# Kernel tuning notes

Hardware: AMD Instinct MI355X
Metric: run time of the kernel (lower is better)

## Reference

```python
import jax, jax.numpy as jnp
import numpy as np

N = 50000      # nodes
E = 800000     # edges (before self loops)
F_IN = 16      # n_input_features
PRE = 32       # n_channels_preproc
C = 128        # n_channels
GH = 32        # edge_gate_hidden_dim
L = 5          # n_gnn_layers (tied weights)


def setup_inputs() -> dict:
    key = jax.random.key(0)
    ks = jax.random.split(key, 16)
    def w(k, shape):
        return jax.random.normal(k, shape, jnp.float32) * 0.05
    return dict(
        x=jax.random.normal(ks[0], (N, F_IN), jnp.float32),
        edge_index=jax.random.randint(ks[1], (2, E), 0, N),
        edge_attr=jax.random.normal(ks[2], (E, 1), jnp.float32),
        W_pre=w(ks[3], (F_IN, PRE)), b_pre=jnp.zeros((PRE,), jnp.float32),
        W_init=w(ks[4], (PRE, C)), b_init=jnp.zeros((C,), jnp.float32),
        W_g1=w(ks[5], (2 * C + 1, GH)), b_g1=jnp.zeros((GH,), jnp.float32),
        W_g2=w(ks[6], (GH, 1)), b_g2=jnp.zeros((1,), jnp.float32),
        W_z=w(ks[7], (2 * C, C)), b_z=jnp.zeros((C,), jnp.float32),
        W_r=w(ks[8], (2 * C, C)), b_r=jnp.zeros((C,), jnp.float32),
        W_h=w(ks[9], (2 * C, C)), b_h=jnp.zeros((C,), jnp.float32),
        W_f1=w(ks[10], (2 * C, C)), b_f1=jnp.zeros((C,), jnp.float32),
        W_f2=w(ks[11], (C, 2)), b_f2=jnp.zeros((2,), jnp.float32),
    )


def reference(x, edge_index, edge_attr,
              W_pre, b_pre, W_init, b_init,
              W_g1, b_g1, W_g2, b_g2,
              W_z, b_z, W_r, b_r, W_h, b_h,
              W_f1, b_f1, W_f2, b_f2):
    n = x.shape[0]
    # add self loops (fill_value=0.0 for edge_attr)
    sl = jnp.arange(n)
    row = jnp.concatenate([edge_index[0], sl])   # source (x_j)
    col = jnp.concatenate([edge_index[1], sl])   # target (x_i), aggregation index
    ea = jnp.concatenate([edge_attr, jnp.zeros((n, 1), x.dtype)], axis=0)
    # symmetric normalization from in-degree (degree of col, incl. self loops)
    deg = jax.ops.segment_sum(jnp.ones(col.shape[0], x.dtype), col, num_segments=n)
    dis = jnp.where(deg > 0, deg ** -0.5, 0.0)
    norm = (dis[row] * dis[col])[:, None]        # [E', 1]

    # preproc + initial node transform
    h = jax.nn.relu(x @ W_pre + b_pre)
    h0 = jax.nn.relu(h @ W_init + b_init)
    h = h0

    for _ in range(L):  # tied GGNN layers
        x_i = h[col]                              # gather target feats  [E', C]
        x_j = h[row]                              # gather source feats  [E', C]
        g_in = jnp.concatenate([x_i, x_j, ea], axis=-1)          # [E', 2C+1]
        gate = jax.nn.sigmoid(jax.nn.relu(g_in @ W_g1 + b_g1) @ W_g2 + b_g2)
        msg = gate * (norm * x_j)                                  # [E', C]
        aggr = jax.ops.segment_sum(msg, col, num_segments=n)       # scatter-add
        # GRU-style update
        za = jnp.concatenate([h, aggr], axis=-1)                   # [N, 2C]
        z = jax.nn.sigmoid(za @ W_z + b_z)
        r = jax.nn.sigmoid(za @ W_r + b_r)
        hc = jax.nn.relu(jnp.concatenate([r * h, aggr], axis=-1) @ W_h + b_h)
        h = (1.0 - z) * h + z * hc

    out = jnp.concatenate([h0, h], axis=-1)       # [N, 2C]
    out = jax.nn.relu(out @ W_f1 + b_f1)
    return out @ W_f2 + b_f2                      # [N, 2] logits (output_activation='none')
```

## Files before the change

### kernel.cpp

```cpp
#include <hip/hip_runtime.h>
#include <math.h>

#define NODES 50000
#define NEDGES 800000
#define ETOT (NEDGES + NODES)
#define FIN 16
#define PRE 32
#define C 128
#define GH 32
#define LAYERS 5
#define RECS 160
#define SCB 64
#define SCT 256
#define SCCH ((NODES + SCB*SCT - 1) / (SCB*SCT))

typedef _Float16 f16;
typedef f16 f16x8 __attribute__((ext_vector_type(8)));
typedef f16 f16x4 __attribute__((ext_vector_type(4)));
typedef f16 f16x2 __attribute__((ext_vector_type(2)));
typedef float f32x4 __attribute__((ext_vector_type(4)));

__device__ __forceinline__ float sigmoidf_(float x) { return 1.0f / (1.0f + __expf(-x)); }

__device__ __forceinline__ int swz_off(int row, int bytecol, int stride) {
    return row * stride + ((((bytecol) >> 4) ^ (row & 7)) << 4) + (bytecol & 15);
}

__device__ __forceinline__ int bperm(int c) { return 4 * (c & 7) + (c >> 3); }

__global__ void k_degree(const int* __restrict__ col, float* __restrict__ deg) {
    int e = blockIdx.x * blockDim.x + threadIdx.x;
    if (e < NEDGES) atomicAdd(&deg[col[e]], 1.0f);
}

__global__ __launch_bounds__(SCT) void k_scan1(const float* __restrict__ deg, int* __restrict__ bsum) {
    __shared__ int ws4[SCT / 64];
    int b = blockIdx.x, t = threadIdx.x;
    int lane = t & 63, wv = t >> 6;
    int base = (b * SCT + t) * SCCH;
    int sum = 0;
#pragma unroll
    for (int j = 0; j < SCCH; j++) {
        int i = base + j;
        if (i < NODES) sum += (int)deg[i] + 1;
    }
#pragma unroll
    for (int off = 32; off > 0; off >>= 1) sum += __shfl_xor(sum, off, 64);
    if (lane == 0) ws4[wv] = sum;
    __syncthreads();
    if (t == 0) {
        int tot = 0;
#pragma unroll
        for (int j = 0; j < SCT / 64; j++) tot += ws4[j];
        bsum[b] = tot;
    }
}

__global__ __launch_bounds__(64) void k_scan2(const int* __restrict__ bsum, int* __restrict__ bscan,
                                              int* __restrict__ start) {
    int t = threadIdx.x;
    int v = (t < SCB) ? bsum[t] : 0;
    int x = v;
#pragma unroll
    for (int off = 1; off < 64; off <<= 1) {
        int tt = __shfl_up(x, off, 64);
        if (t >= off) x += tt;
    }
    if (t < SCB) bscan[t] = x - v;
    if (t == SCB - 1) start[NODES] = x;
}

__global__ __launch_bounds__(SCT) void k_scan3(
    float* __restrict__ deg_dis, const int* __restrict__ bscan,
    int* __restrict__ start, int* __restrict__ cursor) {
    __shared__ int woff[SCT / 64];
    int b = blockIdx.x, t = threadIdx.x;
    int lane = t & 63, wv = t >> 6;
    int base = (b * SCT + t) * SCCH;
    int v[SCCH]; int sum = 0;
#pragma unroll
    for (int j = 0; j < SCCH; j++) {
        int i = base + j;
        v[j] = (i < NODES) ? (int)deg_dis[i] + 1 : 0;
        sum += v[j];
    }
    int x = sum;
#pragma unroll
    for (int off = 1; off < 64; off <<= 1) {
        int tt = __shfl_up(x, off, 64);
        if (lane >= off) x += tt;
    }
    int texcl = x - sum;
    if (lane == 63) woff[wv] = x;
    __syncthreads();
    int wbase = 0;
    for (int j = 0; j < wv; j++) wbase += woff[j];
    int run = bscan[b] + wbase + texcl;
#pragma unroll
    for (int j = 0; j < SCCH; j++) {
        int i = base + j;
        if (i < NODES) {
            start[i] = run; cursor[i] = run;
            deg_dis[i] = rsqrtf((float)v[j]);
        }
        run += v[j];
    }
}

__global__ __launch_bounds__(256) void k_csr(
    const int* __restrict__ eidx, const float* __restrict__ eattr,
    int* __restrict__ cursor,
    int* __restrict__ row_sorted, float* __restrict__ ea_sorted) {
    int e = blockIdx.x * blockDim.x + threadIdx.x;
    if (e >= ETOT) return;
    int r, ci; float ea;
    if (e < NEDGES) { r = eidx[e]; ci = eidx[NEDGES + e]; ea = eattr[e]; }
    else            { r = ci = e - NEDGES; ea = 0.0f; }
    int slot = atomicAdd(&cursor[ci], 1);
    row_sorted[slot] = r;
    ea_sorted[slot] = ea;
}

__global__ __launch_bounds__(256) void k_prep_w(
    const float* __restrict__ Wz, const float* __restrict__ Wr, const float* __restrict__ Wh,
    const float* __restrict__ Wg1, const float* __restrict__ Wf1,
    f16* __restrict__ WcatF, f16* __restrict__ WhtopF, f16* __restrict__ Wg1F,
    f16* __restrict__ Wf1F) {
    int t = blockIdx.x * 256 + threadIdx.x;
    int l = t & 63;
    int lr = l & 15, lh = l >> 4;
    if (t < 24 * 8 * 64) {
        int idx = t >> 6; int nt = idx >> 3, ks = idx & 7;
        int wv = nt / 6, ntl = nt % 6;
        int grp = ntl >> 1, pr = ntl & 1;
        int ncol = (2 * wv + pr) * 16 + lr;
        f16x8 v;
#pragma unroll
        for (int j = 0; j < 8; j++) {
            int k = ks * 32 + lh * 8 + j;
            float x;
            if (grp == 0)      x = Wz[k * 128 + ncol];
            else if (grp == 1) x = Wr[k * 128 + ncol];
            else               x = (k >= 128) ? Wh[k * 128 + ncol] : 0.0f;
            v[j] = (f16)x;
        }
        *(f16x8*)(WcatF + (size_t)t * 8) = v;
    } else if (t < 24 * 8 * 64 + 8 * 4 * 64) {
        int t2 = t - 24 * 8 * 64;
        int idx = t2 >> 6; int nt = idx >> 2, ks = idx & 3;
        int n = nt * 16 + lr;
        f16x8 v;
#pragma unroll
        for (int j = 0; j < 8; j++) {
            int k = ks * 32 + lh * 8 + j;
            v[j] = (f16)Wh[k * 128 + n];
        }
        *(f16x8*)(WhtopF + (size_t)t2 * 8) = v;
    } else if (t < 24 * 8 * 64 + 8 * 4 * 64 + 4 * 4 * 64) {
        int t3 = t - (24 * 8 * 64 + 8 * 4 * 64);
        int idx = t3 >> 6; int nt = idx >> 2, ks = idx & 3;
        int cg = nt * 16 + lr;
        f16x8 v;
#pragma unroll
        for (int j = 0; j < 8; j++) {
            int k = ks * 32 + lh * 8 + j;
            v[j] = (f16)((cg < 32) ? Wg1[k * GH + cg] : Wg1[(128 + k) * GH + (cg - 32)]);
        }
        *(f16x8*)(Wg1F + (size_t)t3 * 8) = v;
    } else if (t < 24 * 8 * 64 + 8 * 4 * 64 + 4 * 4 * 64 + 8 * 8 * 64) {
        int t4 = t - (24 * 8 * 64 + 8 * 4 * 64 + 4 * 4 * 64);
        int idx = t4 >> 6; int nt = idx >> 3, ks = idx & 7;
        int n = nt * 16 + lr;
        f16x8 v;
#pragma unroll
        for (int j = 0; j < 8; j++) {
            int k = ks * 32 + lh * 8 + j;
            v[j] = (f16)Wf1[k * 128 + n];
        }
        *(f16x8*)(Wf1F + (size_t)t4 * 8) = v;
    }
}

__global__ __launch_bounds__(256) void k_preproc(
    const float* __restrict__ x, const float* __restrict__ Wpre, const float* __restrict__ bpre,
    const float* __restrict__ Winit, const float* __restrict__ binit,
    f16* __restrict__ h0_16, f16* __restrict__ h16) {
    __shared__ float sWpre[FIN * PRE], sbpre[PRE], sWinit[PRE * C], sbinit[C];
    for (int i = threadIdx.x; i < FIN * PRE; i += blockDim.x) sWpre[i] = Wpre[i];
    for (int i = threadIdx.x; i < PRE; i += blockDim.x) sbpre[i] = bpre[i];
    for (int i = threadIdx.x; i < PRE * C; i += blockDim.x) sWinit[i] = Winit[i];
    for (int i = threadIdx.x; i < C; i += blockDim.x) sbinit[i] = binit[i];
    __syncthreads();
    int wave = (blockIdx.x * blockDim.x + threadIdx.x) >> 6;
    int lane = threadIdx.x & 63;
    if (wave >= NODES) return;
    float xk = (lane < FIN) ? x[(size_t)wave * FIN + lane] : 0.0f;
    float pre = (lane < PRE) ? sbpre[lane] : 0.0f;
#pragma unroll
    for (int i = 0; i < FIN; i++) {
        float xi = __shfl(xk, i, 64);
        pre = fmaf(xi, (lane < PRE) ? sWpre[i * PRE + lane] : 0.0f, pre);
    }
    pre = fmaxf(pre, 0.0f);
    int c = lane * 2;
    float a0 = sbinit[c], a1 = sbinit[c + 1];
#pragma unroll
    for (int j = 0; j < PRE; j++) {
        float pj = __shfl(pre, j, 64);
        a0 = fmaf(pj, sWinit[j * C + c], a0);
        a1 = fmaf(pj, sWinit[j * C + c + 1], a1);
    }
    a0 = fmaxf(a0, 0.0f); a1 = fmaxf(a1, 0.0f);
    f16x2 o; o[0] = (f16)a0; o[1] = (f16)a1;
    *(f16x2*)&h0_16[(size_t)wave * C + c] = o;
    *(f16x2*)&h16[(size_t)wave * C + c] = o;
}

__global__ __launch_bounds__(256) void k_gate0_mfma(
    const f16* __restrict__ h16, const float* __restrict__ dis,
    const f16* __restrict__ Wg1F, const float* __restrict__ bg1,
    float* __restrict__ A, f16* __restrict__ rec) {
    __shared__ f16 za[32 * 128];
    char* zaB = (char*)za;
    int tid = threadIdx.x;
    int l = tid & 63, w = tid >> 6;
    int lr = l & 15, lh = l >> 4;
    int n0 = blockIdx.x * 32;

    for (int p = tid; p < 32 * 16; p += 256) {
        int row = p >> 4, seg = p & 15;
        int gn = n0 + row;
        f16x8 v = {};
        if (gn < NODES) v = *(const f16x8*)(h16 + (size_t)gn * C + seg * 8);
        *(f16x8*)(zaB + swz_off(row, seg * 16, 256)) = v;
        if (gn < NODES) {
            float dn = dis[gn];
            f16x8 od;
#pragma unroll
            for (int j = 0; j < 8; j++) od[j] = (f16)((float)v[j] * dn);
            *(f16x8*)(rec + (size_t)gn * RECS + 32 + seg * 8) = od;
        }
    }
    __syncthreads();

    f32x4 acc3[2];
#pragma unroll
    for (int rt = 0; rt < 2; rt++)
#pragma unroll
        for (int j = 0; j < 4; j++) acc3[rt][j] = 0.0f;
#pragma unroll
    for (int ks = 0; ks < 4; ks++) {
        int kk = ks * 32 + lh * 8;
        f16x8 a0 = *(const f16x8*)(zaB + swz_off(lr,      kk * 2, 256));
        f16x8 a1 = *(const f16x8*)(zaB + swz_off(lr + 16, kk * 2, 256));
        f16x8 b = *(const f16x8*)(Wg1F + ((size_t)(w * 4 + ks) * 64 + l) * 8);
        acc3[0] = __builtin_amdgcn_mfma_f32_16x16x32_f16(a0, b, acc3[0], 0, 0, 0);
        acc3[1] = __builtin_amdgcn_mfma_f32_16x16x32_f16(a1, b, acc3[1], 0, 0, 0);
    }
    int col3 = w * 16 + lr;
#pragma unroll
    for (int rt = 0; rt < 2; rt++)
#pragma unroll
        for (int j = 0; j < 4; j++) {
            int row = rt * 16 + lh * 4 + j;
            int gn = n0 + row;
            if (gn < NODES) {
                float v = acc3[rt][j];
                if (col3 < 32) A[(size_t)gn * GH + bperm(col3)] = v + bg1[col3];
                else           rec[(size_t)gn * RECS + bperm(col3 - 32)] = (f16)v;
            }
        }
}

__global__ __launch_bounds__(256) void k_msg(
    const int* __restrict__ start, const int* __restrict__ row_sorted,
    const float* __restrict__ ea_sorted, const float* __restrict__ dis,
    const float* __restrict__ A, const f16* __restrict__ rec,
    const float* __restrict__ Wg1, const float* __restrict__ Wg2, const float* __restrict__ bg2,
    f16* __restrict__ aggr16) {
    int wid = (blockIdx.x * blockDim.x + threadIdx.x) >> 6;
    int lane = threadIdx.x & 63;
    if (wid >= NODES) return;
    int k8 = lane & 7;
    int q = lane >> 3;
    int s0 = start[wid], s1 = start[wid + 1];
    float4 a4 = *(const float4*)(A + (size_t)wid * GH + k8 * 4);
    const float* wg1e = Wg1 + 2 * C * GH;
    float wea0 = wg1e[k8], wea1 = wg1e[k8 + 8], wea2 = wg1e[k8 + 16], wea3 = wg1e[k8 + 24];
    float w20 = Wg2[k8], w21 = Wg2[k8 + 8], w22 = Wg2[k8 + 16], w23 = Wg2[k8 + 24];
    float b2 = bg2[0];
    float dci = dis[wid];
    float acc[16];
#pragma unroll
    for (int j = 0; j < 16; j++) acc[j] = 0.0f;

    int s = s0 + q;
    f16x8 ha0 = {}, hb0 = {};
    f16x4 bb0 = {};
    float ea0 = 0.0f;
    if (s < s1) {
        int r = row_sorted[s];
        ea0 = ea_sorted[s];
        const f16* rr = rec + (size_t)r * RECS;
        bb0 = *(const f16x4*)(rr + k8 * 4);
        ha0 = *(const f16x8*)(rr + 32 + k8 * 16);
        hb0 = *(const f16x8*)(rr + 32 + k8 * 16 + 8);
    }
    while (s < s1) {
        int s2 = s + 8;
        f16x8 ha1 = {}, hb1 = {};
        f16x4 bb1 = {};
        float ea1 = 0.0f;
        if (s2 < s1) {
            int r = row_sorted[s2];
            ea1 = ea_sorted[s2];
            const f16* rr = rec + (size_t)r * RECS;
            bb1 = *(const f16x4*)(rr + k8 * 4);
            ha1 = *(const f16x8*)(rr + 32 + k8 * 16);
            hb1 = *(const f16x8*)(rr + 32 + k8 * 16 + 8);
        }
        float t0 = fmaxf(a4.x + (float)bb0[0] + ea0 * wea0, 0.0f);
        float t1 = fmaxf(a4.y + (float)bb0[1] + ea0 * wea1, 0.0f);
        float t2 = fmaxf(a4.z + (float)bb0[2] + ea0 * wea2, 0.0f);
        float t3 = fmaxf(a4.w + (float)bb0[3] + ea0 * wea3, 0.0f);
        float p = t0 * w20;
        p = fmaf(t1, w21, p);
        p = fmaf(t2, w22, p);
        p = fmaf(t3, w23, p);
        p += __shfl_xor(p, 4, 8);
        p += __shfl_xor(p, 2, 8);
        p += __shfl_xor(p, 1, 8);
        float coef = sigmoidf_(p + b2);
#pragma unroll
        for (int j = 0; j < 8; j++) {
            acc[j]     = fmaf(coef, (float)ha0[j], acc[j]);
            acc[8 + j] = fmaf(coef, (float)hb0[j], acc[8 + j]);
        }
        ha0 = ha1; hb0 = hb1; bb0 = bb1; ea0 = ea1;
        s = s2;
    }
#pragma unroll
    for (int j = 0; j < 16; j++) {
        acc[j] += __shfl_xor(acc[j], 8, 64);
        acc[j] += __shfl_xor(acc[j], 16, 64);
        acc[j] += __shfl_xor(acc[j], 32, 64);
    }
    if (lane < 8) {
        f16x8 o1, o2;
#pragma unroll
        for (int j = 0; j < 8; j++) { o1[j] = (f16)(acc[j] * dci); o2[j] = (f16)(acc[8 + j] * dci); }
        *(f16x8*)(aggr16 + (size_t)wid * C + k8 * 16) = o1;
        *(f16x8*)(aggr16 + (size_t)wid * C + k8 * 16 + 8) = o2;
    }
}

__global__ __launch_bounds__(256) void k_update_mfma(
    f16* __restrict__ h16, const f16* __restrict__ aggr16, const float* __restrict__ dis,
    f16* __restrict__ rec,
    const f16* __restrict__ WcatF, const f16* __restrict__ WhtopF, const f16* __restrict__ Wg1F,
    const float* __restrict__ bz, const float* __restrict__ br, const float* __restrict__ bh,
    const float* __restrict__ bg1,
    float* __restrict__ A) {
    __shared__ f16 za[32 * 256];
    __shared__ f16 rhbuf[32 * 128];
    char* zaB = (char*)za;
    char* rhB = (char*)rhbuf;
    int tid = threadIdx.x;
    int l = tid & 63, w = tid >> 6;
    int lr = l & 15, lh = l >> 4;
    int n0 = blockIdx.x * 32;

    for (int p = tid; p < 32 * 16; p += 256) {
        int row = p >> 4, seg = p & 15;
        int gn = n0 + row;
        f16x8 v = {};
        if (gn < NODES) v = *(const f16x8*)(h16 + (size_t)gn * C + seg * 8);
        *(f16x8*)(zaB + swz_off(row, seg * 16, 512)) = v;
    }
    for (int p = tid; p < 32 * 16; p += 256) {
        int row = p >> 4, seg = p & 15;
        int gn = n0 + row;
        f16x8 v = {};
        if (gn < NODES) v = *(const f16x8*)(aggr16 + (size_t)gn * C + seg * 8);
        *(f16x8*)(zaB + swz_off(row, 256 + seg * 16, 512)) = v;
    }
    __syncthreads();

    f32x4 acc[2][6];
#pragma unroll
    for (int rt = 0; rt < 2; rt++)
#pragma unroll
        for (int n = 0; n < 6; n++)
#pragma unroll
            for (int j = 0; j < 4; j++) acc[rt][n][j] = 0.0f;
#pragma unroll
    for (int ks = 0; ks < 8; ks++) {
        int kk = ks * 32 + lh * 8;
        f16x8 a0 = *(const f16x8*)(zaB + swz_off(lr,      kk * 2, 512));
        f16x8 a1 = *(const f16x8*)(zaB + swz_off(lr + 16, kk * 2, 512));
#pragma unroll
        for (int ntl = 0; ntl < 6; ntl++) {
            f16x8 b = *(const f16x8*)(WcatF + ((size_t)((w * 6 + ntl) * 8 + ks) * 64 + l) * 8);
            acc[0][ntl] = __builtin_amdgcn_mfma_f32_16x16x32_f16(a0, b, acc[0][ntl], 0, 0, 0);
            acc[1][ntl] = __builtin_amdgcn_mfma_f32_16x16x32_f16(a1, b, acc[1][ntl], 0, 0, 0);
        }
    }

    float zreg[2][2][4];
#pragma unroll
    for (int rt = 0; rt < 2; rt++)
#pragma unroll
        for (int pr = 0; pr < 2; pr++) {
            int cg = (2 * w + pr) * 16 + lr;
#pragma unroll
            for (int j = 0; j < 4; j++) {
                int row = rt * 16 + lh * 4 + j;
                zreg[rt][pr][j] = sigmoidf_(acc[rt][pr][j] + bz[cg]);
                float rv = sigmoidf_(acc[rt][2 + pr][j] + br[cg]);
                float hv = (float)*(const f16*)(zaB + swz_off(row, cg * 2, 512));
                *(f16*)(rhB + swz_off(row, cg * 2, 256)) = (f16)(rv * hv);
            }
        }
    __syncthreads();

    f32x4 acc2[2][2];
#pragma unroll
    for (int rt = 0; rt < 2; rt++)
#pragma unroll
        for (int pr = 0; pr < 2; pr++) {
            int cg = (2 * w + pr) * 16 + lr;
#pragma unroll
            for (int j = 0; j < 4; j++)
                acc2[rt][pr][j] = acc[rt][4 + pr][j] + bh[cg];
        }
#pragma unroll
    for (int ks = 0; ks < 4; ks++) {
        int kk = ks * 32 + lh * 8;
        f16x8 a0 = *(const f16x8*)(rhB + swz_off(lr,      kk * 2, 256));
        f16x8 a1 = *(const f16x8*)(rhB + swz_off(lr + 16, kk * 2, 256));
#pragma unroll
        for (int pr = 0; pr < 2; pr++) {
            f16x8 b = *(const f16x8*)(WhtopF + ((size_t)((w * 2 + pr) * 4 + ks) * 64 + l) * 8);
            acc2[0][pr] = __builtin_amdgcn_mfma_f32_16x16x32_f16(a0, b, acc2[0][pr], 0, 0, 0);
            acc2[1][pr] = __builtin_amdgcn_mfma_f32_16x16x32_f16(a1, b, acc2[1][pr], 0, 0, 0);
        }
    }

#pragma unroll
    for (int rt = 0; rt < 2; rt++)
#pragma unroll
        for (int pr = 0; pr < 2; pr++) {
            int cg = (2 * w + pr) * 16 + lr;
#pragma unroll
            for (int j = 0; j < 4; j++) {
                int row = rt * 16 + lh * 4 + j;
                int gn = n0 + row;
                float hc = fmaxf(acc2[rt][pr][j], 0.0f);
                float z = zreg[rt][pr][j];
                float hold = (float)*(const f16*)(zaB + swz_off(row, cg * 2, 512));
                float hn = (1.0f - z) * hold + z * hc;
                if (gn < NODES) {
                    h16[(size_t)gn * C + cg] = (f16)hn;
                    rec[(size_t)gn * RECS + 32 + cg] = (f16)(hn * dis[gn]);
                }
                *(f16*)(zaB + swz_off(row, cg * 2, 512)) = (f16)hn;
            }
        }
    __syncthreads();

    f32x4 acc3[2];
#pragma unroll
    for (int rt = 0; rt < 2; rt++)
#pragma unroll
        for (int j = 0; j < 4; j++) acc3[rt][j] = 0.0f;
#pragma unroll
    for (int ks = 0; ks < 4; ks++) {
        int kk = ks * 32 + lh * 8;
        f16x8 a0 = *(const f16x8*)(zaB + swz_off(lr,      kk * 2, 512));
        f16x8 a1 = *(const f16x8*)(zaB + swz_off(lr + 16, kk * 2, 512));
        f16x8 b = *(const f16x8*)(Wg1F + ((size_t)(w * 4 + ks) * 64 + l) * 8);
        acc3[0] = __builtin_amdgcn_mfma_f32_16x16x32_f16(a0, b, acc3[0], 0, 0, 0);
        acc3[1] = __builtin_amdgcn_mfma_f32_16x16x32_f16(a1, b, acc3[1], 0, 0, 0);
    }
    int col3 = w * 16 + lr;
#pragma unroll
    for (int rt = 0; rt < 2; rt++)
#pragma unroll
        for (int j = 0; j < 4; j++) {
            int row = rt * 16 + lh * 4 + j;
            int gn = n0 + row;
            if (gn < NODES) {
                float v = acc3[rt][j];
                if (col3 < 32) A[(size_t)gn * GH + bperm(col3)] = v + bg1[col3];
                else           rec[(size_t)gn * RECS + bperm(col3 - 32)] = (f16)v;
            }
        }
}

__global__ __launch_bounds__(256) void k_final_mfma(
    const f16* __restrict__ h0_16, const f16* __restrict__ h16,
    const f16* __restrict__ Wf1F, const float* __restrict__ bf1,
    const float* __restrict__ Wf2, const float* __restrict__ bf2,
    float* __restrict__ out) {
    __shared__ float fs[32][132];
    char* zaB = (char*)&fs[0][0];
    int tid = threadIdx.x;
    int l = tid & 63, w = tid >> 6;
    int lr = l & 15, lh = l >> 4;
    int n0 = blockIdx.x * 32;

    for (int p = tid; p < 32 * 16; p += 256) {
        int row = p >> 4, seg = p & 15;
        int gn = n0 + row;
        f16x8 v = {};
        if (gn < NODES) v = *(const f16x8*)(h0_16 + (size_t)gn * C + seg * 8);
        *(f16x8*)(zaB + swz_off(row, seg * 16, 512)) = v;
    }
    for (int p = tid; p < 32 * 16; p += 256) {
        int row = p >> 4, seg = p & 15;
        int gn = n0 + row;
        f16x8 v = {};
        if (gn < NODES) v = *(const f16x8*)(h16 + (size_t)gn * C + seg * 8);
        *(f16x8*)(zaB + swz_off(row, 256 + seg * 16, 512)) = v;
    }
    __syncthreads();

    f32x4 acc[2][2];
#pragma unroll
    for (int rt = 0; rt < 2; rt++)
#pragma unroll
        for (int n = 0; n < 2; n++)
#pragma unroll
            for (int j = 0; j < 4; j++) acc[rt][n][j] = 0.0f;
#pragma unroll
    for (int ks = 0; ks < 8; ks++) {
        int kk = ks * 32 + lh * 8;
        f16x8 a0 = *(const f16x8*)(zaB + swz_off(lr,      kk * 2, 512));
        f16x8 a1 = *(const f16x8*)(zaB + swz_off(lr + 16, kk * 2, 512));
#pragma unroll
        for (int ntl = 0; ntl < 2; ntl++) {
            f16x8 b = *(const f16x8*)(Wf1F + ((size_t)((w * 2 + ntl) * 8 + ks) * 64 + l) * 8);
            acc[0][ntl] = __builtin_amdgcn_mfma_f32_16x16x32_f16(a0, b, acc[0][ntl], 0, 0, 0);
            acc[1][ntl] = __builtin_amdgcn_mfma_f32_16x16x32_f16(a1, b, acc[1][ntl], 0, 0, 0);
        }
    }
    __syncthreads();

#pragma unroll
    for (int rt = 0; rt < 2; rt++)
#pragma unroll
        for (int ntl = 0; ntl < 2; ntl++) {
            int cg = (w * 2 + ntl) * 16 + lr;
#pragma unroll
            for (int j = 0; j < 4; j++) {
                int row = rt * 16 + lh * 4 + j;
                fs[row][cg] = fmaxf(acc[rt][ntl][j] + bf1[cg], 0.0f);
            }
        }
    __syncthreads();

    if (tid < 64) {
        int n = tid >> 1, o = tid & 1;
        int gn = n0 + n;
        if (gn < NODES) {
            float a = bf2[o];
#pragma unroll 16
            for (int c = 0; c < C; c++) a = fmaf(fs[n][c], Wf2[c * 2 + o], a);
            out[(size_t)gn * 2 + o] = a;
        }
    }
}

extern "C" void kernel_launch(void* const* d_in, const int* in_sizes, int n_in,
                              void* d_out, int out_size, void* d_ws, size_t ws_size,
                              hipStream_t stream) {
    const float* x    = (const float*)d_in[0];
    const int*   eidx = (const int*)d_in[1];
    const float* eattr= (const float*)d_in[2];
    const float* Wpre = (const float*)d_in[3];  const float* bpre = (const float*)d_in[4];
    const float* Winit= (const float*)d_in[5];  const float* binit= (const float*)d_in[6];
    const float* Wg1  = (const float*)d_in[7];  const float* bg1  = (const float*)d_in[8];
    const float* Wg2  = (const float*)d_in[9];  const float* bg2  = (const float*)d_in[10];
    const float* Wz   = (const float*)d_in[11]; const float* bz   = (const float*)d_in[12];
    const float* Wr   = (const float*)d_in[13]; const float* br   = (const float*)d_in[14];
    const float* Wh   = (const float*)d_in[15]; const float* bh   = (const float*)d_in[16];
    const float* Wf1  = (const float*)d_in[17]; const float* bf1  = (const float*)d_in[18];
    const float* Wf2  = (const float*)d_in[19]; const float* bf2  = (const float*)d_in[20];
    float* out = (float*)d_out;

    float* ws  = (float*)d_ws;
    float* dis = ws;
    float* A   = dis + NODES;
    int*   start = (int*)(A + (size_t)NODES * GH);
    int*   cursor = start + NODES + 1;
    int*   bsum  = cursor + NODES + 1;
    int*   bscan = bsum + SCB;
    int*   row_sorted = bscan + SCB;
    float* ea_sorted  = (float*)(row_sorted + ETOT);
    size_t f16_base = (size_t)((ea_sorted + ETOT) - ws);
    f16_base = (f16_base + 3) & ~(size_t)3;
    f16* h0_16  = (f16*)(ws + f16_base);
    f16* h16    = h0_16 + (size_t)NODES * C;
    f16* rec    = h16 + (size_t)NODES * C;
    f16* aggr16 = rec + (size_t)NODES * RECS;
    f16* WcatF  = aggr16 + (size_t)NODES * C;
    f16* WhtopF = WcatF + 24 * 8 * 64 * 8;
    f16* Wg1F   = WhtopF + 8 * 4 * 64 * 8;
    f16* Wf1F   = Wg1F + 4 * 4 * 64 * 8;
    size_t f16_total = (size_t)NODES * (C + C + RECS + C) + (24 * 8 + 8 * 4 + 4 * 4 + 8 * 8) * 64 * 8;
    const size_t REQ = (f16_base + (f16_total + 1) / 2) * sizeof(float);
    if (ws_size < REQ) return;

    hipMemsetAsync(dis, 0, NODES * sizeof(float), stream);
    k_degree<<<(NEDGES + 255) / 256, 256, 0, stream>>>(eidx + NEDGES, dis);
    k_scan1<<<SCB, SCT, 0, stream>>>(dis, bsum);
    k_scan2<<<1, 64, 0, stream>>>(bsum, bscan, start);
    k_scan3<<<SCB, SCT, 0, stream>>>(dis, bscan, start, cursor);
    k_csr<<<(ETOT + 255) / 256, 256, 0, stream>>>(eidx, eattr, cursor, row_sorted, ea_sorted);
    k_prep_w<<<(24 * 8 * 64 + 8 * 4 * 64 + 4 * 4 * 64 + 8 * 8 * 64 + 255) / 256, 256, 0, stream>>>(
        Wz, Wr, Wh, Wg1, Wf1, WcatF, WhtopF, Wg1F, Wf1F);
    k_preproc<<<(NODES * 64 + 255) / 256, 256, 0, stream>>>(x, Wpre, bpre, Winit, binit, h0_16, h16);
    k_gate0_mfma<<<(NODES + 31) / 32, 256, 0, stream>>>(h16, dis, Wg1F, bg1, A, rec);

    for (int l = 0; l < LAYERS; l++) {
        k_msg<<<(NODES * 64 + 255) / 256, 256, 0, stream>>>(
            start, row_sorted, ea_sorted, dis, A, rec, Wg1, Wg2, bg2, aggr16);
        k_update_mfma<<<(NODES + 31) / 32, 256, 0, stream>>>(
            h16, aggr16, dis, rec, WcatF, WhtopF, Wg1F, bz, br, bh, bg1, A);
    }
    k_final_mfma<<<(NODES + 31) / 32, 256, 0, stream>>>(h0_16, h16, Wf1F, bf1, Wf2, bf2, out);
}
```

Before: 631.8 us.

## Fuse preprocessing MLP into gate-0 kernel using MFMA

Replaces the scalar wave-per-node preprocessing kernel with MFMA-based x@W_pre and pre@W_init computed inside the layer-0 gate kernel. h0/h16 are written from shared memory, so gate-0 no longer rereads h16 from global memory, and one kernel launch is removed. The W_pre and W_init weights are now packed into fp16 fragment layout in k_prep_w. This adds fp16 rounding of x and of the intermediate activations.

```diff
diff --git a/kernel.cpp b/kernel.cpp
--- a/kernel.cpp
+++ b/kernel.cpp
@@ -25,6 +25,9 @@
 __device__ __forceinline__ int swz_off(int row, int bytecol, int stride) {
     return row * stride + ((((bytecol) >> 4) ^ (row & 7)) << 4) + (bytecol & 15);
 }
+__device__ __forceinline__ int ps_off(int row, int bytecol) {
+    return row * 64 + ((((bytecol) >> 4) ^ (row & 3)) << 4) + (bytecol & 15);
+}
 
 __device__ __forceinline__ int bperm(int c) { return 4 * (c & 7) + (c >> 3); }
 
@@ -124,8 +127,9 @@
 __global__ __launch_bounds__(256) void k_prep_w(
     const float* __restrict__ Wz, const float* __restrict__ Wr, const float* __restrict__ Wh,
     const float* __restrict__ Wg1, const float* __restrict__ Wf1,
+    const float* __restrict__ Wpre, const float* __restrict__ Winit,
     f16* __restrict__ WcatF, f16* __restrict__ WhtopF, f16* __restrict__ Wg1F,
-    f16* __restrict__ Wf1F) {
+    f16* __restrict__ Wf1F, f16* __restrict__ WpreF, f16* __restrict__ WinitF) {
     int t = blockIdx.x * 256 + threadIdx.x;
     int l = t & 63;
     int lr = l & 15, lh = l >> 4;
@@ -178,62 +182,107 @@
             v[j] = (f16)Wf1[k * 128 + n];
         }
         *(f16x8*)(Wf1F + (size_t)t4 * 8) = v;
-    }
-}
-
-__global__ __launch_bounds__(256) void k_preproc(
-    const float* __restrict__ x, const float* __restrict__ Wpre, const float* __restrict__ bpre,
-    const float* __restrict__ Winit, const float* __restrict__ binit,
-    f16* __restrict__ h0_16, f16* __restrict__ h16) {
-    __shared__ float sWpre[FIN * PRE], sbpre[PRE], sWinit[PRE * C], sbinit[C];
-    for (int i = threadIdx.x; i < FIN * PRE; i += blockDim.x) sWpre[i] = Wpre[i];
-    for (int i = threadIdx.x; i < PRE; i += blockDim.x) sbpre[i] = bpre[i];
-    for (int i = threadIdx.x; i < PRE * C; i += blockDim.x) sWinit[i] = Winit[i];
-    for (int i = threadIdx.x; i < C; i += blockDim.x) sbinit[i] = binit[i];
-    __syncthreads();
-    int wave = (blockIdx.x * blockDim.x + threadIdx.x) >> 6;
-    int lane = threadIdx.x & 63;
-    if (wave >= NODES) return;
-    float xk = (lane < FIN) ? x[(size_t)wave * FIN + lane] : 0.0f;
-    float pre = (lane < PRE) ? sbpre[lane] : 0.0f;
-#pragma unroll
-    for (int i = 0; i < FIN; i++) {
-        float xi = __shfl(xk, i, 64);
-        pre = fmaf(xi, (lane < PRE) ? sWpre[i * PRE + lane] : 0.0f, pre);
-    }
-    pre = fmaxf(pre, 0.0f);
-    int c = lane * 2;
-    float a0 = sbinit[c], a1 = sbinit[c + 1];
-#pragma unroll
-    for (int j = 0; j < PRE; j++) {
-        float pj = __shfl(pre, j, 64);
-        a0 = fmaf(pj, sWinit[j * C + c], a0);
-        a1 = fmaf(pj, sWinit[j * C + c + 1], a1);
-    }
-    a0 = fmaxf(a0, 0.0f); a1 = fmaxf(a1, 0.0f);
-    f16x2 o; o[0] = (f16)a0; o[1] = (f16)a1;
-    *(f16x2*)&h0_16[(size_t)wave * C + c] = o;
-    *(f16x2*)&h16[(size_t)wave * C + c] = o;
-}
-
-__global__ __launch_bounds__(256) void k_gate0_mfma(
-    const f16* __restrict__ h16, const float* __restrict__ dis,
+    } else if (t < 19456 + 2 * 64) {
+        int t5 = t - 19456;
+        int nt = t5 >> 6;
+        f16x8 v;
+#pragma unroll
+        for (int j = 0; j < 8; j++) {
+            int k = lh * 8 + j;
+            v[j] = (k < FIN) ? (f16)Wpre[k * PRE + nt * 16 + lr] : (f16)0.0f;
+        }
+        *(f16x8*)(WpreF + (size_t)t5 * 8) = v;
+    } else if (t < 19456 + 128 + 8 * 64) {
+        int t6 = t - 19456 - 128;
+        int nt = t6 >> 6;
+        f16x8 v;
+#pragma unroll
+        for (int j = 0; j < 8; j++) {
+            int k = lh * 8 + j;
+            v[j] = (f16)Winit[k * C + nt * 16 + lr];
+        }
+        *(f16x8*)(WinitF + (size_t)t6 * 8) = v;
+    }
+}
+
+__global__ __launch_bounds__(256) void k_pre_gate(
+    const float* __restrict__ x, const float* __restrict__ bpre, const float* __restrict__ binit,
+    const float* __restrict__ dis,
+    const f16* __restrict__ WpreF, const f16* __restrict__ WinitF,
     const f16* __restrict__ Wg1F, const float* __restrict__ bg1,
-    float* __restrict__ A, f16* __restrict__ rec) {
+    f16* __restrict__ h0_16, f16* __restrict__ h16, f16* __restrict__ rec,
+    float* __restrict__ A) {
+    __shared__ f16 ps[32 * 32];
     __shared__ f16 za[32 * 128];
+    char* psB = (char*)ps;
     char* zaB = (char*)za;
     int tid = threadIdx.x;
     int l = tid & 63, w = tid >> 6;
     int lr = l & 15, lh = l >> 4;
     int n0 = blockIdx.x * 32;
+    int rt0 = w >> 1, ct = w & 1;
+
+    f16x8 xa = {};
+    {
+        int gn = n0 + rt0 * 16 + lr;
+        if (gn < NODES && lh < 2) {
+            float4 xv0 = *(const float4*)(x + (size_t)gn * FIN + lh * 8);
+            float4 xv1 = *(const float4*)(x + (size_t)gn * FIN + lh * 8 + 4);
+            xa[0] = (f16)xv0.x; xa[1] = (f16)xv0.y; xa[2] = (f16)xv0.z; xa[3] = (f16)xv0.w;
+            xa[4] = (f16)xv1.x; xa[5] = (f16)xv1.y; xa[6] = (f16)xv1.z; xa[7] = (f16)xv1.w;
+        }
+    }
+    f16x8 bA = *(const f16x8*)(WpreF + ((size_t)ct * 64 + l) * 8);
+    f32x4 accA; accA[0] = accA[1] = accA[2] = accA[3] = 0.0f;
+    accA = __builtin_amdgcn_mfma_f32_16x16x32_f16(xa, bA, accA, 0, 0, 0);
+    {
+        float bp = bpre[ct * 16 + lr];
+#pragma unroll
+        for (int j = 0; j < 4; j++) {
+            int row = rt0 * 16 + lh * 4 + j;
+            float v = fmaxf(accA[j] + bp, 0.0f);
+            *(f16*)(psB + ps_off(row, (ct * 16 + lr) * 2)) = (f16)v;
+        }
+    }
+    __syncthreads();
+
+    f16x8 pa0 = *(const f16x8*)(psB + ps_off(lr, lh * 16));
+    f16x8 pa1 = *(const f16x8*)(psB + ps_off(lr + 16, lh * 16));
+    f32x4 accB[2][2];
+#pragma unroll
+    for (int rt = 0; rt < 2; rt++)
+#pragma unroll
+        for (int ntl = 0; ntl < 2; ntl++)
+#pragma unroll
+            for (int j = 0; j < 4; j++) accB[rt][ntl][j] = 0.0f;
+#pragma unroll
+    for (int ntl = 0; ntl < 2; ntl++) {
+        f16x8 b = *(const f16x8*)(WinitF + ((size_t)((w * 2 + ntl) * 64 + l)) * 8);
+        accB[0][ntl] = __builtin_amdgcn_mfma_f32_16x16x32_f16(pa0, b, accB[0][ntl], 0, 0, 0);
+        accB[1][ntl] = __builtin_amdgcn_mfma_f32_16x16x32_f16(pa1, b, accB[1][ntl], 0, 0, 0);
+    }
+#pragma unroll
+    for (int rt = 0; rt < 2; rt++)
+#pragma unroll
+        for (int ntl = 0; ntl < 2; ntl++) {
+            int cg = (w * 2 + ntl) * 16 + lr;
+            float bi = binit[cg];
+#pragma unroll
+            for (int j = 0; j < 4; j++) {
+                int row = rt * 16 + lh * 4 + j;
+                float v = fmaxf(accB[rt][ntl][j] + bi, 0.0f);
+                *(f16*)(zaB + swz_off(row, cg * 2, 256)) = (f16)v;
+            }
+        }
+    __syncthreads();
 
     for (int p = tid; p < 32 * 16; p += 256) {
         int row = p >> 4, seg = p & 15;
         int gn = n0 + row;
-        f16x8 v = {};
-        if (gn < NODES) v = *(const f16x8*)(h16 + (size_t)gn * C + seg * 8);
-        *(f16x8*)(zaB + swz_off(row, seg * 16, 256)) = v;
         if (gn < NODES) {
+            f16x8 v = *(const f16x8*)(zaB + swz_off(row, seg * 16, 256));
+            *(f16x8*)(h0_16 + (size_t)gn * C + seg * 8) = v;
+            *(f16x8*)(h16 + (size_t)gn * C + seg * 8) = v;
             float dn = dis[gn];
             f16x8 od;
 #pragma unroll
@@ -241,7 +290,6 @@
             *(f16x8*)(rec + (size_t)gn * RECS + 32 + seg * 8) = od;
         }
     }
-    __syncthreads();
 
     f32x4 acc3[2];
 #pragma unroll
@@ -607,7 +655,10 @@
     f16* WhtopF = WcatF + 24 * 8 * 64 * 8;
     f16* Wg1F   = WhtopF + 8 * 4 * 64 * 8;
     f16* Wf1F   = Wg1F + 4 * 4 * 64 * 8;
-    size_t f16_total = (size_t)NODES * (C + C + RECS + C) + (24 * 8 + 8 * 4 + 4 * 4 + 8 * 8) * 64 * 8;
+    f16* WpreF  = Wf1F + 8 * 8 * 64 * 8;
+    f16* WinitF = WpreF + 2 * 64 * 8;
+    size_t f16_total = (size_t)NODES * (C + C + RECS + C)
+                     + (24 * 8 + 8 * 4 + 4 * 4 + 8 * 8 + 2 + 8) * 64 * 8;
     const size_t REQ = (f16_base + (f16_total + 1) / 2) * sizeof(float);
     if (ws_size < REQ) return;
 
@@ -617,10 +668,10 @@
     k_scan2<<<1, 64, 0, stream>>>(bsum, bscan, start);
     k_scan3<<<SCB, SCT, 0, stream>>>(dis, bscan, start, cursor);
     k_csr<<<(ETOT + 255) / 256, 256, 0, stream>>>(eidx, eattr, cursor, row_sorted, ea_sorted);
-    k_prep_w<<<(24 * 8 * 64 + 8 * 4 * 64 + 4 * 4 * 64 + 8 * 8 * 64 + 255) / 256, 256, 0, stream>>>(
-        Wz, Wr, Wh, Wg1, Wf1, WcatF, WhtopF, Wg1F, Wf1F);
-    k_preproc<<<(NODES * 64 + 255) / 256, 256, 0, stream>>>(x, Wpre, bpre, Winit, binit, h0_16, h16);
-    k_gate0_mfma<<<(NODES + 31) / 32, 256, 0, stream>>>(h16, dis, Wg1F, bg1, A, rec);
+    k_prep_w<<<(19456 + 128 + 512 + 255) / 256, 256, 0, stream>>>(
+        Wz, Wr, Wh, Wg1, Wf1, Wpre, Winit, WcatF, WhtopF, Wg1F, Wf1F, WpreF, WinitF);
+    k_pre_gate<<<(NODES + 31) / 32, 256, 0, stream>>>(
+        x, bpre, binit, dis, WpreF, WinitF, Wg1F, bg1, h0_16, h16, rec, A);
 
     for (int l = 0; l < LAYERS; l++) {
         k_msg<<<(NODES * 64 + 255) / 256, 256, 0, stream>>>(
```

After: 580.1 us. -8.2%, faster.
